# Performance work log

Hardware: AMD Instinct MI355X
Metric: run time of the kernel (lower is better)

The kernel has to match this reference:

```python
import jax, jax.numpy as jnp
import numpy as np

CUTOFF = 0.05

def _freq_filter(x_chw, filter_type):
    # x_chw: [C,H,W] = batch element 0, detached in the original (stop_gradient)
    x = jax.lax.stop_gradient(x_chw)
    C, H, W = x.shape
    a = jnp.abs(x)
    mn = a.min(axis=(1, 2), keepdims=True)
    ptp = a.max(axis=(1, 2), keepdims=True) - mn
    # np.uint8(255*(a-mn)/ptp): values in [0,255], cast truncates -> floor
    q = jnp.floor(255.0 * (a - mn) / ptp)
    f = jnp.fft.fftshift(jnp.fft.fft2(q), axes=(-2, -1))
    crow, ccol = H // 2, W // 2
    dr, dc = int(CUTOFF * crow), int(CUTOFF * ccol)
    m = jnp.zeros((H, W), dtype=q.dtype)
    m = m.at[crow - dr:crow + dr, ccol - dc:ccol + dc].set(1.0)
    if filter_type == 'low_pass':
        m = 1.0 - m  # note: original 'low_pass' actually removes low freqs
    out = jnp.abs(jnp.fft.ifft2(jnp.fft.ifftshift(f * m, axes=(-2, -1))))
    return out.astype(x_chw.dtype)  # [C,H,W]

def _conv1x1(x, w, b):
    # x: [B,C,H,W], w: [O,C], b: [O]
    return jnp.einsum('oc,bchw->bohw', w, x) + b[None, :, None, None]

def setup_inputs() -> dict:
    key = jax.random.key(0)
    ks = jax.random.split(key, 7)
    B, C, H, W = 1, 256, 96, 96
    fuse = jax.random.normal(ks[0], (B, C, H, W), dtype=jnp.float32)
    s = 1.0 / np.sqrt(C)
    Wq = jax.random.normal(ks[1], (C, C), dtype=jnp.float32) * s
    bq = jax.random.normal(ks[2], (C,), dtype=jnp.float32) * 0.01
    Wk = jax.random.normal(ks[3], (C, C), dtype=jnp.float32) * s
    bk = jax.random.normal(ks[4], (C,), dtype=jnp.float32) * 0.01
    Wv = jax.random.normal(ks[5], (C, C), dtype=jnp.float32) * s
    bv = jax.random.normal(ks[6], (C,), dtype=jnp.float32) * 0.01
    return {"fuse": fuse, "Wq": Wq, "bq": bq, "Wk": Wk, "bk": bk, "Wv": Wv, "bv": bv}

def reference(fuse, Wq, bq, Wk, bk, Wv, bv):
    B, C, H, W = fuse.shape
    scale = 1.0 / (C ** 0.5)
    # frequency-filtered maps (computed from batch 0, broadcast to all batches)
    FQ = jnp.broadcast_to(_freq_filter(fuse[0], 'high_pass'), fuse.shape)
    FK = jnp.broadcast_to(_freq_filter(fuse[0], 'low_pass'), fuse.shape)
    fuse_Query = _conv1x1(FQ, Wq, bq).reshape(B, C, H * W)     # [B,C,HW]
    fuse_Q_mask = fuse_Query.reshape(B * H, C * W)             # [B*H, C*W]
    fuse_Query_t = jnp.transpose(fuse_Query, (0, 2, 1))        # [B,HW,C]
    fuse_Key = _conv1x1(FK, Wk, bk).reshape(B, C, H * W)       # [B,C,HW]
    Fuse_Q_mask = jnp.max(fuse_Q_mask, axis=0, keepdims=True)  # [1, C*W]
    mask_KQ = jnp.einsum('bnc,bcm->bnm', fuse_Query_t, fuse_Key) * scale  # [B,HW,HW]
    mask_KQ = jax.nn.softmax(mask_KQ, axis=0)  # softmax over batch dim (as in original)
    mask_KQ = jnp.max(mask_KQ, axis=1)                         # [B,HW]
    mask_KQ = mask_KQ.reshape(-1, W)                           # [B*H, W]
    mask_KQ = jnp.max(mask_KQ, axis=-1, keepdims=True)         # [B*H, 1]
    mask = (mask_KQ @ Fuse_Q_mask).reshape(B, C, H, W)
    fuse_Value = _conv1x1(fuse, Wv, bv)
    return fuse_Value + fuse_Value * mask
```

## Files before the change

### kernel.cpp

```cpp
#include <hip/hip_runtime.h>
#include <math.h>

#define CCH 256
#define HW  9216
#define CW  24576
#define TWO_PI 6.28318530717958647692f

typedef __attribute__((ext_vector_type(8))) short short8;
typedef __attribute__((ext_vector_type(4))) float f32x4;

__device__ inline unsigned short f2bf(float f) {
    unsigned u = __float_as_uint(f);
    unsigned r = (u + 0x7FFFu + ((u >> 16) & 1u)) >> 16;
    return (unsigned short)r;
}

__global__ __launch_bounds__(768) void k_pre(const float* __restrict__ x,
                                             const float* __restrict__ Wq,
                                             const float* __restrict__ Wv,
                                             short8* __restrict__ Wqt,
                                             short8* __restrict__ Wvt,
                                             unsigned* __restrict__ FQm,
                                             float* __restrict__ Fg) {
    __shared__ float qa[HW];
    __shared__ float cs[96][2];
    __shared__ float Gp[8][96][5];
    __shared__ float Gs[96][6];
    __shared__ float red[24];
    __shared__ float s_mn, s_ptp;
    int bid = blockIdx.x, t = threadIdx.x;

    if (bid >= 256) {
        int widx = bid - 256;
        if (t < 256) {
            const float* src = (widx >= 32) ? Wv : Wq;
            short8* dst = (widx >= 32) ? Wvt : Wqt;
            int cidx = (widx & 31) * 256 + t;
            int ot = cidx >> 11, kc = (cidx >> 6) & 31, m = cidx & 63;
            const float* s = src + (ot * 64 + m) * 256 + kc * 8;
            short8 v;
            #pragma unroll
            for (int e = 0; e < 8; ++e) v[e] = (short)f2bf(s[e]);
            dst[cidx] = v;
        }
        return;
    }

    int c = bid;
    if (t < 96) FQm[c * 96 + t] = 0u;
    const float* xp = x + c * HW;
    if (t < 96) { float a = TWO_PI * (float)t / 96.0f; cs[t][0] = cosf(a); cs[t][1] = sinf(a); }
    float lo = 1e30f, hi = 0.f;
    #pragma unroll
    for (int i = 0; i < 12; ++i) {
        float a = fabsf(xp[t + i * 768]);
        qa[t + i * 768] = a;
        lo = fminf(lo, a);
        hi = fmaxf(hi, a);
    }
    #pragma unroll
    for (int d = 32; d; d >>= 1) {
        lo = fminf(lo, __shfl_xor(lo, d, 64));
        hi = fmaxf(hi, __shfl_xor(hi, d, 64));
    }
    if ((t & 63) == 0) { red[t >> 6] = lo; red[12 + (t >> 6)] = hi; }
    __syncthreads();
    if (t == 0) {
        lo = red[0]; hi = red[12];
        #pragma unroll
        for (int i = 1; i < 12; ++i) { lo = fminf(lo, red[i]); hi = fmaxf(hi, red[12 + i]); }
        s_mn = lo; s_ptp = hi - lo;
    }
    __syncthreads();
    float mn = s_mn, ptp = s_ptp;

    {
        int xx = t % 96, h = t / 96;
        float g0r = 0, g0i = 0, g1r = 0, g1i = 0, g2 = 0;
        for (int y = h * 12; y < h * 12 + 12; ++y) {
            float q = floorf(255.0f * (qa[y * 96 + xx] - mn) / ptp);
            float c1 = cs[y][0], s1 = cs[y][1];
            float c2 = c1 * c1 - s1 * s1, s2 = 2.0f * c1 * s1;
            g0r += q * c2; g0i += q * s2;
            g1r += q * c1; g1i += q * s1;
            g2  += q;
        }
        Gp[h][xx][0] = g0r; Gp[h][xx][1] = g0i;
        Gp[h][xx][2] = g1r; Gp[h][xx][3] = g1i;
        Gp[h][xx][4] = g2;
    }
    __syncthreads();
    if (t < 96) {
        #pragma unroll
        for (int j = 0; j < 5; ++j) {
            float s = 0.f;
            #pragma unroll
            for (int h = 0; h < 8; ++h) s += Gp[h][t][j];
            Gs[t][j] = s;
        }
        Gs[t][5] = 0.f;
    }
    __syncthreads();
    if (t < 64) {
        int coef = t >> 2, qq = t & 3;
        int ky = coef >> 2, kx = coef & 3;
        float fr = 0, fi = 0;
        for (int xx = qq * 24; xx < qq * 24 + 24; ++xx) {
            float c1 = cs[xx][0], s1 = cs[xx][1];
            float er, ei;
            if (kx == 0)      { er = c1 * c1 - s1 * s1; ei = 2.0f * c1 * s1; }
            else if (kx == 1) { er = c1; ei = s1; }
            else if (kx == 2) { er = 1.f; ei = 0.f; }
            else              { er = c1; ei = -s1; }
            float gr, gi;
            if (ky == 0)      { gr = Gs[xx][0]; gi = Gs[xx][1]; }
            else if (ky == 1) { gr = Gs[xx][2]; gi = Gs[xx][3]; }
            else if (ky == 2) { gr = Gs[xx][4]; gi = 0.f; }
            else              { gr = Gs[xx][2]; gi = -Gs[xx][3]; }
            fr += gr * er - gi * ei;
            fi += gr * ei + gi * er;
        }
        fr += __shfl_xor(fr, 1, 64); fr += __shfl_xor(fr, 2, 64);
        fi += __shfl_xor(fi, 1, 64); fi += __shfl_xor(fi, 2, 64);
        if (qq == 0) {
            Fg[c * 32 + 2 * coef]     = fr;
            Fg[c * 32 + 2 * coef + 1] = fi;
        }
    }
}

__global__ __launch_bounds__(256) void k_gemm1(const short8* __restrict__ Wt,
                                               const float* __restrict__ Fg,
                                               const float* __restrict__ bias,
                                               unsigned* __restrict__ FQm) {
    __shared__ short8 As[2048];
    __shared__ short8 Bs[2048];
    __shared__ float Rs[2048][2];
    int tid = threadIdx.x;
    int pt_ = blockIdx.x, ot = blockIdx.y;
    const short8* wsrc = Wt + ot * 2048;
    #pragma unroll
    for (int i = 0; i < 8; ++i) As[i * 256 + tid] = wsrc[i * 256 + tid];

    int p0 = pt_ * 64;
    int y0 = p0 / 96;
    {
        int yi = (tid >> 2) & 1, kx = tid & 3, cb = tid >> 3;
        float ay = TWO_PI * (float)(y0 + yi) / 96.0f;
        float cyv = cosf(ay), syv = sinf(ay);
        float cy2 = cyv * cyv - syv * syv, sy2 = 2.f * cyv * syv;
        float Ur[4] = { cy2, cyv, 1.f, cyv };
        float Ui[4] = { -sy2, -syv, 0.f, syv };
        #pragma unroll
        for (int i = 0; i < 8; ++i) {
            int cc = cb + i * 32;
            float rr = 0.f, ri = 0.f;
            #pragma unroll
            for (int ky = 0; ky < 4; ++ky) {
                float fr = Fg[cc * 32 + 2 * (ky * 4 + kx)];
                float fi = Fg[cc * 32 + 2 * (ky * 4 + kx) + 1];
                rr += fr * Ur[ky] - fi * Ui[ky];
                ri += fr * Ui[ky] + fi * Ur[ky];
            }
            Rs[cc * 8 + yi * 4 + kx][0] = rr;
            Rs[cc * 8 + yi * 4 + kx][1] = ri;
        }
    }
    __syncthreads();
    const float inv = 1.0f / 9216.0f;
    #pragma unroll
    for (int i = 0; i < 8; ++i) {
        int si = i * 256 + tid;
        int kcg = si >> 6, n = si & 63;
        int p = p0 + n;
        int y = p / 96, xx = p - y * 96;
        int yi = y - y0;
        float axv = TWO_PI * (float)xx / 96.0f;
        float cxv = cosf(axv), sxv = sinf(axv);
        float cx2 = cxv * cxv - sxv * sxv, sx2 = 2.f * cxv * sxv;
        float Tr[4] = { cx2, cxv, 1.f, cxv };
        float Ti[4] = { -sx2, -sxv, 0.f, sxv };
        short8 vv;
        #pragma unroll
        for (int e = 0; e < 8; ++e) {
            int rb = (kcg * 8 + e) * 8 + yi * 4;
            float ar = 0.f, ai = 0.f;
            #pragma unroll
            for (int kx = 0; kx < 4; ++kx) {
                float rr = Rs[rb + kx][0], ri = Rs[rb + kx][1];
                ar += rr * Tr[kx] - ri * Ti[kx];
                ai += rr * Ti[kx] + ri * Tr[kx];
            }
            vv[e] = (short)f2bf(sqrtf(ar * ar + ai * ai) * inv);
        }
        Bs[si] = vv;
    }
    __syncthreads();

    int l = tid & 63, w = tid >> 6;
    int wr = w >> 1, wc = w & 1;
    int l15 = l & 15, quad = l >> 4;
    f32x4 acc[2][2] = {};
    int abase = wr * 32 + l15;
    int bbase = wc * 32 + l15;
    #pragma unroll
    for (int s = 0; s < 8; ++s) {
        int kc = s * 4 + quad;
        short8 a0 = As[kc * 64 + abase];
        short8 a1 = As[kc * 64 + abase + 16];
        short8 b0 = Bs[kc * 64 + bbase];
        short8 b1 = Bs[kc * 64 + bbase + 16];
        acc[0][0] = __builtin_amdgcn_mfma_f32_16x16x32_bf16(a0, b0, acc[0][0], 0, 0, 0);
        acc[0][1] = __builtin_amdgcn_mfma_f32_16x16x32_bf16(a0, b1, acc[0][1], 0, 0, 0);
        acc[1][0] = __builtin_amdgcn_mfma_f32_16x16x32_bf16(a1, b0, acc[1][0], 0, 0, 0);
        acc[1][1] = __builtin_amdgcn_mfma_f32_16x16x32_bf16(a1, b1, acc[1][1], 0, 0, 0);
    }
    #pragma unroll
    for (int ni = 0; ni < 2; ++ni) {
        #pragma unroll
        for (int r = 0; r < 4; ++r) {
            int o_lo = ot * 64 + wr * 32 + quad * 4 + r;
            float v = fmaxf(acc[0][ni][r] + bias[o_lo], acc[1][ni][r] + bias[o_lo + 16]);
            v = fmaxf(v, __shfl_xor(v, 32, 64));
            if (quad < 2) {
                int p = pt_ * 64 + wc * 32 + ni * 16 + l15;
                int k = ((quad * 4 + r) & 7) * HW + p;
                if (k >= CW) k -= CW;
                if (k >= CW) k -= CW;
                unsigned u = __float_as_uint(v);
                unsigned key = (u & 0x80000000u) ? ~u : (u | 0x80000000u);
                atomicMax(&FQm[k], key);
            }
        }
    }
}

__global__ __launch_bounds__(256) void k_gemm2(const short8* __restrict__ Wt,
                                               const float* __restrict__ x,
                                               const float* __restrict__ bias,
                                               const unsigned* __restrict__ FQm,
                                               float* __restrict__ out) {
    __shared__ short8 As[2048];
    __shared__ short8 Bs[2048];
    int tid = threadIdx.x;
    int pt_ = blockIdx.x, ot = blockIdx.y;
    const short8* wsrc = Wt + ot * 2048;
    #pragma unroll
    for (int i = 0; i < 8; ++i) As[i * 256 + tid] = wsrc[i * 256 + tid];

    int p0 = pt_ * 64;
    #pragma unroll
    for (int i = 0; i < 8; ++i) {
        int si = i * 256 + tid;
        int KC = si >> 6, n = si & 63;
        const float* xb = x + (size_t)(KC * 8) * HW + p0 + n;
        short8 v;
        #pragma unroll
        for (int e = 0; e < 8; ++e) v[e] = (short)f2bf(xb[(size_t)e * HW]);
        Bs[si] = v;
    }
    __syncthreads();

    int l = tid & 63, w = tid >> 6;
    int wr = w >> 1, wc = w & 1;
    int l15 = l & 15, quad = l >> 4;
    f32x4 acc[2][2] = {};
    int abase = wr * 32 + l15;
    int bbase = wc * 32 + l15;
    #pragma unroll
    for (int s = 0; s < 8; ++s) {
        int kc = s * 4 + quad;
        short8 a0 = As[kc * 64 + abase];
        short8 a1 = As[kc * 64 + abase + 16];
        short8 b0 = Bs[kc * 64 + bbase];
        short8 b1 = Bs[kc * 64 + bbase + 16];
        acc[0][0] = __builtin_amdgcn_mfma_f32_16x16x32_bf16(a0, b0, acc[0][0], 0, 0, 0);
        acc[0][1] = __builtin_amdgcn_mfma_f32_16x16x32_bf16(a0, b1, acc[0][1], 0, 0, 0);
        acc[1][0] = __builtin_amdgcn_mfma_f32_16x16x32_bf16(a1, b0, acc[1][0], 0, 0, 0);
        acc[1][1] = __builtin_amdgcn_mfma_f32_16x16x32_bf16(a1, b1, acc[1][1], 0, 0, 0);
    }
    #pragma unroll
    for (int mi = 0; mi < 2; ++mi) {
        #pragma unroll
        for (int ni = 0; ni < 2; ++ni) {
            #pragma unroll
            for (int r = 0; r < 4; ++r) {
                int o = ot * 64 + wr * 32 + mi * 16 + quad * 4 + r;
                int p = pt_ * 64 + wc * 32 + ni * 16 + l15;
                int k = ((quad * 4 + r) & 7) * HW + p;
                if (k >= CW) k -= CW;
                if (k >= CW) k -= CW;
                unsigned key = FQm[k];
                unsigned ub = (key & 0x80000000u) ? (key ^ 0x80000000u) : ~key;
                float m = __uint_as_float(ub);
                float v = acc[mi][ni][r] + bias[o];
                out[(size_t)o * HW + p] = v * (1.0f + m);
            }
        }
    }
}

extern "C" void kernel_launch(void* const* d_in, const int* in_sizes, int n_in,
                              void* d_out, int out_size, void* d_ws, size_t ws_size,
                              hipStream_t stream) {
    const float* fuse = (const float*)d_in[0];
    const float* Wq   = (const float*)d_in[1];
    const float* bq   = (const float*)d_in[2];
    const float* Wv   = (const float*)d_in[5];
    const float* bv   = (const float*)d_in[6];
    float* out = (float*)d_out;

    char* ws = (char*)d_ws;
    unsigned* FQm = (unsigned*)(ws);
    float*    Fg  = (float*)(ws + 98304);
    short8*   Wqt = (short8*)(ws + 131072);
    short8*   Wvt = (short8*)(ws + 262144);

    k_pre<<<320, 768, 0, stream>>>(fuse, Wq, Wv, Wqt, Wvt, FQm, Fg);
    k_gemm1<<<dim3(144, 4), 256, 0, stream>>>(Wqt, Fg, bq, FQm);
    k_gemm2<<<dim3(144, 4), 256, 0, stream>>>(Wvt, fuse, bv, FQm, out);
}
```

Baseline: 115.6 us.

## Merge Q and V GEMMs into one launch and apply mask in separate pass

Fuses the Q-projection GEMM (with FFT reconstruction and atomic max) and the V-projection GEMM into a single 1152-block launch, so both run concurrently instead of V waiting for Q. Because V blocks can no longer read the finished mask, they write the unmasked value to the output, and a new elementwise kernel then reads the output back, applies the mask and writes it again. The aim is better GPU fill and one fewer serialized GEMM dependency. The cost is an extra read and write pass over the roughly 9 MB output, plus one more kernel launch.

```diff
diff --git a/kernel.cpp b/kernel.cpp
--- a/kernel.cpp
+++ b/kernel.cpp
@@ -129,71 +129,90 @@
     }
 }
 
-__global__ __launch_bounds__(256) void k_gemm1(const short8* __restrict__ Wt,
-                                               const float* __restrict__ Fg,
-                                               const float* __restrict__ bias,
-                                               unsigned* __restrict__ FQm) {
+__global__ __launch_bounds__(256) void k_gemmQV(const short8* __restrict__ Wqt,
+                                                const short8* __restrict__ Wvt,
+                                                const float* __restrict__ Fg,
+                                                const float* __restrict__ bq,
+                                                const float* __restrict__ bv,
+                                                const float* __restrict__ x,
+                                                unsigned* __restrict__ FQm,
+                                                float* __restrict__ out) {
     __shared__ short8 As[2048];
     __shared__ short8 Bs[2048];
     __shared__ float Rs[2048][2];
     int tid = threadIdx.x;
-    int pt_ = blockIdx.x, ot = blockIdx.y;
-    const short8* wsrc = Wt + ot * 2048;
+    int pt_ = blockIdx.x;
+    bool isQ = blockIdx.y < 4;
+    int ot = isQ ? blockIdx.y : blockIdx.y - 4;
+    const short8* wsrc = (isQ ? Wqt : Wvt) + ot * 2048;
     #pragma unroll
     for (int i = 0; i < 8; ++i) As[i * 256 + tid] = wsrc[i * 256 + tid];
 
     int p0 = pt_ * 64;
-    int y0 = p0 / 96;
-    {
-        int yi = (tid >> 2) & 1, kx = tid & 3, cb = tid >> 3;
-        float ay = TWO_PI * (float)(y0 + yi) / 96.0f;
-        float cyv = cosf(ay), syv = sinf(ay);
-        float cy2 = cyv * cyv - syv * syv, sy2 = 2.f * cyv * syv;
-        float Ur[4] = { cy2, cyv, 1.f, cyv };
-        float Ui[4] = { -sy2, -syv, 0.f, syv };
+    if (isQ) {
+        int y0 = p0 / 96;
+        {
+            int yi = (tid >> 2) & 1, kx = tid & 3, cb = tid >> 3;
+            float ay = TWO_PI * (float)(y0 + yi) / 96.0f;
+            float cyv = cosf(ay), syv = sinf(ay);
+            float cy2 = cyv * cyv - syv * syv, sy2 = 2.f * cyv * syv;
+            float Ur[4] = { cy2, cyv, 1.f, cyv };
+            float Ui[4] = { -sy2, -syv, 0.f, syv };
+            #pragma unroll
+            for (int i = 0; i < 8; ++i) {
+                int cc = cb + i * 32;
+                float rr = 0.f, ri = 0.f;
+                #pragma unroll
+                for (int ky = 0; ky < 4; ++ky) {
+                    float fr = Fg[cc * 32 + 2 * (ky * 4 + kx)];
+                    float fi = Fg[cc * 32 + 2 * (ky * 4 + kx) + 1];
+                    rr += fr * Ur[ky] - fi * Ui[ky];
+                    ri += fr * Ui[ky] + fi * Ur[ky];
+                }
+                Rs[cc * 8 + yi * 4 + kx][0] = rr;
+                Rs[cc * 8 + yi * 4 + kx][1] = ri;
+            }
+        }
+        __syncthreads();
+        const float inv = 1.0f / 9216.0f;
         #pragma unroll
         for (int i = 0; i < 8; ++i) {
-            int cc = cb + i * 32;
-            float rr = 0.f, ri = 0.f;
-            #pragma unroll
-            for (int ky = 0; ky < 4; ++ky) {
-                float fr = Fg[cc * 32 + 2 * (ky * 4 + kx)];
-                float fi = Fg[cc * 32 + 2 * (ky * 4 + kx) + 1];
-                rr += fr * Ur[ky] - fi * Ui[ky];
-                ri += fr * Ui[ky] + fi * Ur[ky];
+            int si = i * 256 + tid;
+            int kcg = si >> 6, n = si & 63;
+            int p = p0 + n;
+            int y = p / 96, xx = p - y * 96;
+            int yi = y - y0;
+            float axv = TWO_PI * (float)xx / 96.0f;
+            float cxv = cosf(axv), sxv = sinf(axv);
+            float cx2 = cxv * cxv - sxv * sxv, sx2 = 2.f * cxv * sxv;
+            float Tr[4] = { cx2, cxv, 1.f, cxv };
+            float Ti[4] = { -sx2, -sxv, 0.f, sxv };
+            short8 vv;
+            #pragma unroll
+            for (int e = 0; e < 8; ++e) {
+                int rb = (kcg * 8 + e) * 8 + yi * 4;
+                float ar = 0.f, ai = 0.f;
+                #pragma unroll
+                for (int kx = 0; kx < 4; ++kx) {
+                    float rr = Rs[rb + kx][0], ri = Rs[rb + kx][1];
+                    ar += rr * Tr[kx] - ri * Ti[kx];
+                    ai += rr * Ti[kx] + ri * Tr[kx];
+                }
+                vv[e] = (short)f2bf(sqrtf(ar * ar + ai * ai) * inv);
             }
-            Rs[cc * 8 + yi * 4 + kx][0] = rr;
-            Rs[cc * 8 + yi * 4 + kx][1] = ri;
-        }
-    }
-    __syncthreads();
-    const float inv = 1.0f / 9216.0f;
-    #pragma unroll
-    for (int i = 0; i < 8; ++i) {
-        int si = i * 256 + tid;
-        int kcg = si >> 6, n = si & 63;
-        int p = p0 + n;
-        int y = p / 96, xx = p - y * 96;
-        int yi = y - y0;
-        float axv = TWO_PI * (float)xx / 96.0f;
-        float cxv = cosf(axv), sxv = sinf(axv);
-        float cx2 = cxv * cxv - sxv * sxv, sx2 = 2.f * cxv * sxv;
-        float Tr[4] = { cx2, cxv, 1.f, cxv };
-        float Ti[4] = { -sx2, -sxv, 0.f, sxv };
-        short8 vv;
-        #pragma unroll
-        for (int e = 0; e < 8; ++e) {
-            int rb = (kcg * 8 + e) * 8 + yi * 4;
-            float ar = 0.f, ai = 0.f;
-            #pragma unroll
-            for (int kx = 0; kx < 4; ++kx) {
-                float rr = Rs[rb + kx][0], ri = Rs[rb + kx][1];
-                ar += rr * Tr[kx] - ri * Ti[kx];
-                ai += rr * Ti[kx] + ri * Tr[kx];
-            }
-            vv[e] = (short)f2bf(sqrtf(ar * ar + ai * ai) * inv);
-        }
-        Bs[si] = vv;
+            Bs[si] = vv;
+        }
+    } else {
+        #pragma unroll
+        for (int i = 0; i < 8; ++i) {
+            int si = i * 256 + tid;
+            int KC = si >> 6, n = si & 63;
+            const float* xb = x + (size_t)(KC * 8) * HW + p0 + n;
+            short8 v;
+            #pragma unroll
+            for (int e = 0; e < 8; ++e) v[e] = (short)f2bf(xb[(size_t)e * HW]);
+            Bs[si] = v;
+        }
     }
     __syncthreads();
 
@@ -215,89 +234,64 @@
         acc[1][0] = __builtin_amdgcn_mfma_f32_16x16x32_bf16(a1, b0, acc[1][0], 0, 0, 0);
         acc[1][1] = __builtin_amdgcn_mfma_f32_16x16x32_bf16(a1, b1, acc[1][1], 0, 0, 0);
     }
-    #pragma unroll
-    for (int ni = 0; ni < 2; ++ni) {
-        #pragma unroll
-        for (int r = 0; r < 4; ++r) {
-            int o_lo = ot * 64 + wr * 32 + quad * 4 + r;
-            float v = fmaxf(acc[0][ni][r] + bias[o_lo], acc[1][ni][r] + bias[o_lo + 16]);
-            v = fmaxf(v, __shfl_xor(v, 32, 64));
-            if (quad < 2) {
-                int p = pt_ * 64 + wc * 32 + ni * 16 + l15;
-                int k = ((quad * 4 + r) & 7) * HW + p;
-                if (k >= CW) k -= CW;
-                if (k >= CW) k -= CW;
-                unsigned u = __float_as_uint(v);
-                unsigned key = (u & 0x80000000u) ? ~u : (u | 0x80000000u);
-                atomicMax(&FQm[k], key);
+
+    if (isQ) {
+        #pragma unroll
+        for (int ni = 0; ni < 2; ++ni) {
+            #pragma unroll
+            for (int r = 0; r < 4; ++r) {
+                int o_lo = ot * 64 + wr * 32 + quad * 4 + r;
+                float v = fmaxf(acc[0][ni][r] + bq[o_lo], acc[1][ni][r] + bq[o_lo + 16]);
+                v = fmaxf(v, __shfl_xor(v, 32, 64));
+                if (quad < 2) {
+                    int p = pt_ * 64 + wc * 32 + ni * 16 + l15;
+                    int k = ((quad * 4 + r) & 7) * HW + p;
+                    if (k >= CW) k -= CW;
+                    if (k >= CW) k -= CW;
+                    unsigned u = __float_as_uint(v);
+                    unsigned key = (u & 0x80000000u) ? ~u : (u | 0x80000000u);
+                    atomicMax(&FQm[k], key);
+                }
             }
         }
-    }
-}
-
-__global__ __launch_bounds__(256) void k_gemm2(const short8* __restrict__ Wt,
-                                               const float* __restrict__ x,
-                                               const float* __restrict__ bias,
-                                               const unsigned* __restrict__ FQm,
-                                               float* __restrict__ out) {
-    __shared__ short8 As[2048];
-    __shared__ short8 Bs[2048];
-    int tid = threadIdx.x;
-    int pt_ = blockIdx.x, ot = blockIdx.y;
-    const short8* wsrc = Wt + ot * 2048;
-    #pragma unroll
-    for (int i = 0; i < 8; ++i) As[i * 256 + tid] = wsrc[i * 256 + tid];
-
-    int p0 = pt_ * 64;
-    #pragma unroll
-    for (int i = 0; i < 8; ++i) {
-        int si = i * 256 + tid;
-        int KC = si >> 6, n = si & 63;
-        const float* xb = x + (size_t)(KC * 8) * HW + p0 + n;
-        short8 v;
-        #pragma unroll
-        for (int e = 0; e < 8; ++e) v[e] = (short)f2bf(xb[(size_t)e * HW]);
-        Bs[si] = v;
-    }
-    __syncthreads();
-
-    int l = tid & 63, w = tid >> 6;
-    int wr = w >> 1, wc = w & 1;
-    int l15 = l & 15, quad = l >> 4;
-    f32x4 acc[2][2] = {};
-    int abase = wr * 32 + l15;
-    int bbase = wc * 32 + l15;
-    #pragma unroll
-    for (int s = 0; s < 8; ++s) {
-        int kc = s * 4 + quad;
-        short8 a0 = As[kc * 64 + abase];
-        short8 a1 = As[kc * 64 + abase + 16];
-        short8 b0 = Bs[kc * 64 + bbase];
-        short8 b1 = Bs[kc * 64 + bbase + 16];
-        acc[0][0] = __builtin_amdgcn_mfma_f32_16x16x32_bf16(a0, b0, acc[0][0], 0, 0, 0);
-        acc[0][1] = __builtin_amdgcn_mfma_f32_16x16x32_bf16(a0, b1, acc[0][1], 0, 0, 0);
-        acc[1][0] = __builtin_amdgcn_mfma_f32_16x16x32_bf16(a1, b0, acc[1][0], 0, 0, 0);
-        acc[1][1] = __builtin_amdgcn_mfma_f32_16x16x32_bf16(a1, b1, acc[1][1], 0, 0, 0);
-    }
-    #pragma unroll
-    for (int mi = 0; mi < 2; ++mi) {
-        #pragma unroll
-        for (int ni = 0; ni < 2; ++ni) {
-            #pragma unroll
-            for (int r = 0; r < 4; ++r) {
-                int o = ot * 64 + wr * 32 + mi * 16 + quad * 4 + r;
-                int p = pt_ * 64 + wc * 32 + ni * 16 + l15;
-                int k = ((quad * 4 + r) & 7) * HW + p;
-                if (k >= CW) k -= CW;
-                if (k >= CW) k -= CW;
-                unsigned key = FQm[k];
-                unsigned ub = (key & 0x80000000u) ? (key ^ 0x80000000u) : ~key;
-                float m = __uint_as_float(ub);
-                float v = acc[mi][ni][r] + bias[o];
-                out[(size_t)o * HW + p] = v * (1.0f + m);
+    } else {
+        #pragma unroll
+        for (int mi = 0; mi < 2; ++mi) {
+            #pragma unroll
+            for (int ni = 0; ni < 2; ++ni) {
+                #pragma unroll
+                for (int r = 0; r < 4; ++r) {
+                    int o = ot * 64 + wr * 32 + mi * 16 + quad * 4 + r;
+                    int p = pt_ * 64 + wc * 32 + ni * 16 + l15;
+                    out[(size_t)o * HW + p] = acc[mi][ni][r] + bv[o];
+                }
             }
         }
     }
+}
+
+__device__ inline float mdecode(unsigned key) {
+    unsigned ub = (key & 0x80000000u) ? (key ^ 0x80000000u) : ~key;
+    return __uint_as_float(ub);
+}
+__global__ __launch_bounds__(256) void k_mask(float* __restrict__ out,
+                                              const unsigned* __restrict__ FQm) {
+    int i = (blockIdx.x * 256 + threadIdx.x) * 8;
+    int o = i / HW;
+    int p = i - o * HW;
+    int k = (o & 7) * HW + p;
+    if (k >= CW) k -= CW;
+    if (k >= CW) k -= CW;
+    float4 v0 = *(const float4*)(out + i);
+    float4 v1 = *(const float4*)(out + i + 4);
+    uint4 k0 = *(const uint4*)(FQm + k);
+    uint4 k1 = *(const uint4*)(FQm + k + 4);
+    v0.x *= 1.0f + mdecode(k0.x); v0.y *= 1.0f + mdecode(k0.y);
+    v0.z *= 1.0f + mdecode(k0.z); v0.w *= 1.0f + mdecode(k0.w);
+    v1.x *= 1.0f + mdecode(k1.x); v1.y *= 1.0f + mdecode(k1.y);
+    v1.z *= 1.0f + mdecode(k1.z); v1.w *= 1.0f + mdecode(k1.w);
+    *(float4*)(out + i)     = v0;
+    *(float4*)(out + i + 4) = v1;
 }
 
 extern "C" void kernel_launch(void* const* d_in, const int* in_sizes, int n_in,
@@ -317,6 +311,6 @@
     short8*   Wvt = (short8*)(ws + 262144);
 
     k_pre<<<320, 768, 0, stream>>>(fuse, Wq, Wv, Wqt, Wvt, FQm, Fg);
-    k_gemm1<<<dim3(144, 4), 256, 0, stream>>>(Wqt, Fg, bq, FQm);
-    k_gemm2<<<dim3(144, 4), 256, 0, stream>>>(Wvt, fuse, bv, FQm, out);
-}
+    k_gemmQV<<<dim3(144, 8), 256, 0, stream>>>(Wqt, Wvt, Fg, bq, bv, fuse, FQm, out);
+    k_mask<<<1152, 256, 0, stream>>>(out, FQm);
+}
```

After: 114.1 us, median of 3. About the same (-1.2%).

## Fuse three kernels into one cooperative persistent kernel with grid syncs

Applied to the files above, without the earlier changes.

Merges the preprocessing, Q-conv mask GEMM and V-conv output GEMM into a single cooperative kernel. Grid-wide syncs separate the phases, and blocks loop over tasks and tiles. The goal is to remove two kernel launch gaps. The preprocessing block shrinks from 768 to 256 threads, so each channel's spectral reduction runs with fewer threads per block. In exchange it adds grid.sync overhead, a fixed grid size, and a per-call occupancy query on the host.

```diff
diff --git a/kernel.cpp b/kernel.cpp
--- a/kernel.cpp
+++ b/kernel.cpp
@@ -1,300 +1,284 @@
 #include <hip/hip_runtime.h>
+#include <hip/hip_cooperative_groups.h>
 #include <math.h>
 
-#define CCH 256
 #define HW  9216
 #define CW  24576
 #define TWO_PI 6.28318530717958647692f
 
+namespace cg = cooperative_groups;
+
 typedef __attribute__((ext_vector_type(8))) short short8;
 typedef __attribute__((ext_vector_type(4))) float f32x4;
 
 __device__ inline unsigned short f2bf(float f) {
     unsigned u = __float_as_uint(f);
-    unsigned r = (u + 0x7FFFu + ((u >> 16) & 1u)) >> 16;
-    return (unsigned short)r;
+    return (unsigned short)((u + 0x7FFFu + ((u >> 16) & 1u)) >> 16);
 }
 
-__global__ __launch_bounds__(768) void k_pre(const float* __restrict__ x,
-                                             const float* __restrict__ Wq,
-                                             const float* __restrict__ Wv,
-                                             short8* __restrict__ Wqt,
-                                             short8* __restrict__ Wvt,
-                                             unsigned* __restrict__ FQm,
-                                             float* __restrict__ Fg) {
-    __shared__ float qa[HW];
-    __shared__ float cs[96][2];
-    __shared__ float Gp[8][96][5];
-    __shared__ float Gs[96][6];
-    __shared__ float red[24];
-    __shared__ float s_mn, s_ptp;
-    int bid = blockIdx.x, t = threadIdx.x;
-
-    if (bid >= 256) {
-        int widx = bid - 256;
-        if (t < 256) {
-            const float* src = (widx >= 32) ? Wv : Wq;
-            short8* dst = (widx >= 32) ? Wvt : Wqt;
-            int cidx = (widx & 31) * 256 + t;
-            int ot = cidx >> 11, kc = (cidx >> 6) & 31, m = cidx & 63;
-            const float* s = src + (ot * 64 + m) * 256 + kc * 8;
+__global__ __launch_bounds__(256, 2) void k_all(const float* __restrict__ x,
+                                                const float* __restrict__ Wq,
+                                                const float* __restrict__ Wv,
+                                                const float* __restrict__ bq,
+                                                const float* __restrict__ bv,
+                                                unsigned* __restrict__ FQm,
+                                                float* __restrict__ Fg,
+                                                short8* __restrict__ Wqt,
+                                                short8* __restrict__ Wvt,
+                                                float* __restrict__ out) {
+    __shared__ __align__(16) char smem[81920];
+    cg::grid_group grid = cg::this_grid();
+    const int bid = blockIdx.x, t = threadIdx.x;
+    const int G = gridDim.x;
+
+    for (int task = bid; task < 368; task += G) {
+        if (task < 256) {
+            float* qa        = (float*)smem;
+            float (*cs)[2]   = (float(*)[2])(smem + 36864);
+            float (*Gp)[96][5] = (float(*)[96][5])(smem + 37632);
+            float (*Gs)[6]   = (float(*)[6])(smem + 41472);
+            float* red       = (float*)(smem + 43776);
+            const float* xp = x + task * HW;
+            if (t < 96) { float a = TWO_PI * (float)t / 96.0f; cs[t][0] = cosf(a); cs[t][1] = sinf(a); }
+            float lo = 1e30f, hi = 0.f;
+            #pragma unroll
+            for (int i = 0; i < 36; ++i) {
+                float a = fabsf(xp[t + i * 256]);
+                qa[t + i * 256] = a;
+                lo = fminf(lo, a); hi = fmaxf(hi, a);
+            }
+            #pragma unroll
+            for (int d = 32; d; d >>= 1) {
+                lo = fminf(lo, __shfl_xor(lo, d, 64));
+                hi = fmaxf(hi, __shfl_xor(hi, d, 64));
+            }
+            if ((t & 63) == 0) { red[t >> 6] = lo; red[4 + (t >> 6)] = hi; }
+            __syncthreads();
+            if (t == 0) {
+                lo = fminf(fminf(red[0], red[1]), fminf(red[2], red[3]));
+                hi = fmaxf(fmaxf(red[4], red[5]), fmaxf(red[6], red[7]));
+                red[8] = lo; red[9] = hi - lo;
+            }
+            __syncthreads();
+            float mn = red[8], ptp = red[9];
+            if (t < 192) {
+                int xx = t % 96, h = t / 96;
+                float g0r = 0, g0i = 0, g1r = 0, g1i = 0, g2 = 0;
+                for (int y = h * 48; y < h * 48 + 48; ++y) {
+                    float q = floorf(255.0f * (qa[y * 96 + xx] - mn) / ptp);
+                    float c1 = cs[y][0], s1 = cs[y][1];
+                    float c2 = c1 * c1 - s1 * s1, s2 = 2.0f * c1 * s1;
+                    g0r += q * c2; g0i += q * s2;
+                    g1r += q * c1; g1i += q * s1;
+                    g2  += q;
+                }
+                Gp[h][xx][0] = g0r; Gp[h][xx][1] = g0i;
+                Gp[h][xx][2] = g1r; Gp[h][xx][3] = g1i;
+                Gp[h][xx][4] = g2;
+            }
+            __syncthreads();
+            if (t < 96) {
+                #pragma unroll
+                for (int j = 0; j < 5; ++j) Gs[t][j] = Gp[0][t][j] + Gp[1][t][j];
+                Gs[t][5] = 0.f;
+            }
+            __syncthreads();
+            if (t < 64) {
+                int coef = t >> 2, qq = t & 3;
+                int ky = coef >> 2, kx = coef & 3;
+                float fr = 0, fi = 0;
+                for (int xx = qq * 24; xx < qq * 24 + 24; ++xx) {
+                    float c1 = cs[xx][0], s1 = cs[xx][1];
+                    float er, ei;
+                    if (kx == 0)      { er = c1 * c1 - s1 * s1; ei = 2.0f * c1 * s1; }
+                    else if (kx == 1) { er = c1; ei = s1; }
+                    else if (kx == 2) { er = 1.f; ei = 0.f; }
+                    else              { er = c1; ei = -s1; }
+                    float gr, gi;
+                    if (ky == 0)      { gr = Gs[xx][0]; gi = Gs[xx][1]; }
+                    else if (ky == 1) { gr = Gs[xx][2]; gi = Gs[xx][3]; }
+                    else if (ky == 2) { gr = Gs[xx][4]; gi = 0.f; }
+                    else              { gr = Gs[xx][2]; gi = -Gs[xx][3]; }
+                    fr += gr * er - gi * ei;
+                    fi += gr * ei + gi * er;
+                }
+                fr += __shfl_xor(fr, 1, 64); fr += __shfl_xor(fr, 2, 64);
+                fi += __shfl_xor(fi, 1, 64); fi += __shfl_xor(fi, 2, 64);
+                if (qq == 0) {
+                    Fg[task * 32 + 2 * coef]     = fr;
+                    Fg[task * 32 + 2 * coef + 1] = fi;
+                }
+            }
+            __syncthreads();
+        } else if (task < 272) {
+            int gi = (task - 256) * 256 + t;
+            #pragma unroll
+            for (int r = 0; r < 4; ++r) {
+                int chunk = gi + r * 4096;
+                const float* src = (chunk < 8192) ? Wq : Wv;
+                short8* dst = (chunk < 8192) ? Wqt : Wvt;
+                int cidx = chunk & 8191;
+                int ot = cidx >> 11, kc = (cidx >> 6) & 31, m = cidx & 63;
+                const float* s = src + (ot * 64 + m) * 256 + kc * 8;
+                short8 v;
+                #pragma unroll
+                for (int e = 0; e < 8; ++e) v[e] = (short)f2bf(s[e]);
+                dst[cidx] = v;
+            }
+        } else {
+            FQm[(task - 272) * 256 + t] = 0u;
+        }
+    }
+    grid.sync();
+
+    short8* As = (short8*)smem;
+    short8* Bs = (short8*)(smem + 32768);
+    float (*Rs)[2] = (float(*)[2])(smem + 65536);
+    const int l = t & 63, w = t >> 6;
+    const int wr = w >> 1, wc = w & 1;
+    const int l15 = l & 15, quad = l >> 4;
+    const int abase = wr * 32 + l15, bbase = wc * 32 + l15;
+
+    for (int tile = bid; tile < 576; tile += G) {
+        __syncthreads();
+        int ot = tile / 144, pt_ = tile % 144;
+        const short8* wsrc = Wqt + ot * 2048;
+        #pragma unroll
+        for (int i = 0; i < 8; ++i) As[i * 256 + t] = wsrc[i * 256 + t];
+        int p0 = pt_ * 64, y0 = p0 / 96;
+        {
+            int yi = (t >> 2) & 1, kx = t & 3, cb = t >> 3;
+            float ay = TWO_PI * (float)(y0 + yi) / 96.0f;
+            float cyv = cosf(ay), syv = sinf(ay);
+            float cy2 = cyv * cyv - syv * syv, sy2 = 2.f * cyv * syv;
+            float Ur[4] = { cy2, cyv, 1.f, cyv };
+            float Ui[4] = { -sy2, -syv, 0.f, syv };
+            #pragma unroll
+            for (int i = 0; i < 8; ++i) {
+                int cc = cb + i * 32;
+                float rr = 0.f, ri = 0.f;
+                #pragma unroll
+                for (int ky = 0; ky < 4; ++ky) {
+                    float fr = Fg[cc * 32 + 2 * (ky * 4 + kx)];
+                    float fi = Fg[cc * 32 + 2 * (ky * 4 + kx) + 1];
+                    rr += fr * Ur[ky] - fi * Ui[ky];
+                    ri += fr * Ui[ky] + fi * Ur[ky];
+                }
+                Rs[cc * 8 + yi * 4 + kx][0] = rr;
+                Rs[cc * 8 + yi * 4 + kx][1] = ri;
+            }
+        }
+        __syncthreads();
+        const float inv = 1.0f / 9216.0f;
+        #pragma unroll
+        for (int i = 0; i < 8; ++i) {
+            int si = i * 256 + t;
+            int kcg = si >> 6, n = si & 63;
+            int p = p0 + n;
+            int y = p / 96, xx = p - y * 96;
+            int yi = y - y0;
+            float axv = TWO_PI * (float)xx / 96.0f;
+            float cxv = cosf(axv), sxv = sinf(axv);
+            float cx2 = cxv * cxv - sxv * sxv, sx2 = 2.f * cxv * sxv;
+            float Tr[4] = { cx2, cxv, 1.f, cxv };
+            float Ti[4] = { -sx2, -sxv, 0.f, sxv };
+            short8 vv;
+            #pragma unroll
+            for (int e = 0; e < 8; ++e) {
+                int rb = (kcg * 8 + e) * 8 + yi * 4;
+                float ar = 0.f, ai = 0.f;
+                #pragma unroll
+                for (int kx2 = 0; kx2 < 4; ++kx2) {
+                    float rr = Rs[rb + kx2][0], ri = Rs[rb + kx2][1];
+                    ar += rr * Tr[kx2] - ri * Ti[kx2];
+                    ai += rr * Ti[kx2] + ri * Tr[kx2];
+                }
+                vv[e] = (short)f2bf(sqrtf(ar * ar + ai * ai) * inv);
+            }
+            Bs[si] = vv;
+        }
+        __syncthreads();
+        f32x4 acc[2][2] = {};
+        #pragma unroll
+        for (int s = 0; s < 8; ++s) {
+            int kc = s * 4 + quad;
+            short8 a0 = As[kc * 64 + abase];
+            short8 a1 = As[kc * 64 + abase + 16];
+            short8 b0 = Bs[kc * 64 + bbase];
+            short8 b1 = Bs[kc * 64 + bbase + 16];
+            acc[0][0] = __builtin_amdgcn_mfma_f32_16x16x32_bf16(a0, b0, acc[0][0], 0, 0, 0);
+            acc[0][1] = __builtin_amdgcn_mfma_f32_16x16x32_bf16(a0, b1, acc[0][1], 0, 0, 0);
+            acc[1][0] = __builtin_amdgcn_mfma_f32_16x16x32_bf16(a1, b0, acc[1][0], 0, 0, 0);
+            acc[1][1] = __builtin_amdgcn_mfma_f32_16x16x32_bf16(a1, b1, acc[1][1], 0, 0, 0);
+        }
+        #pragma unroll
+        for (int ni = 0; ni < 2; ++ni) {
+            #pragma unroll
+            for (int r = 0; r < 4; ++r) {
+                int o_lo = ot * 64 + wr * 32 + quad * 4 + r;
+                float v = fmaxf(acc[0][ni][r] + bq[o_lo], acc[1][ni][r] + bq[o_lo + 16]);
+                v = fmaxf(v, __shfl_xor(v, 32, 64));
+                if (quad < 2) {
+                    int p = pt_ * 64 + wc * 32 + ni * 16 + l15;
+                    int k = ((quad * 4 + r) & 7) * HW + p;
+                    if (k >= CW) k -= CW;
+                    if (k >= CW) k -= CW;
+                    unsigned u = __float_as_uint(v);
+                    unsigned key = (u & 0x80000000u) ? ~u : (u | 0x80000000u);
+                    atomicMax(&FQm[k], key);
+                }
+            }
+        }
+    }
+    grid.sync();
+
+    for (int tile = bid; tile < 576; tile += G) {
+        __syncthreads();
+        int ot = tile / 144, pt_ = tile % 144;
+        const short8* wsrc = Wvt + ot * 2048;
+        #pragma unroll
+        for (int i = 0; i < 8; ++i) As[i * 256 + t] = wsrc[i * 256 + t];
+        int p0 = pt_ * 64;
+        #pragma unroll
+        for (int i = 0; i < 8; ++i) {
+            int si = i * 256 + t;
+            int KC = si >> 6, n = si & 63;
+            const float* xb = x + (size_t)(KC * 8) * HW + p0 + n;
             short8 v;
             #pragma unroll
-            for (int e = 0; e < 8; ++e) v[e] = (short)f2bf(s[e]);
-            dst[cidx] = v;
-        }
-        return;
-    }
-
-    int c = bid;
-    if (t < 96) FQm[c * 96 + t] = 0u;
-    const float* xp = x + c * HW;
-    if (t < 96) { float a = TWO_PI * (float)t / 96.0f; cs[t][0] = cosf(a); cs[t][1] = sinf(a); }
-    float lo = 1e30f, hi = 0.f;
-    #pragma unroll
-    for (int i = 0; i < 12; ++i) {
-        float a = fabsf(xp[t + i * 768]);
-        qa[t + i * 768] = a;
-        lo = fminf(lo, a);
-        hi = fmaxf(hi, a);
-    }
-    #pragma unroll
-    for (int d = 32; d; d >>= 1) {
-        lo = fminf(lo, __shfl_xor(lo, d, 64));
-        hi = fmaxf(hi, __shfl_xor(hi, d, 64));
-    }
-    if ((t & 63) == 0) { red[t >> 6] = lo; red[12 + (t >> 6)] = hi; }
-    __syncthreads();
-    if (t == 0) {
-        lo = red[0]; hi = red[12];
-        #pragma unroll
-        for (int i = 1; i < 12; ++i) { lo = fminf(lo, red[i]); hi = fmaxf(hi, red[12 + i]); }
-        s_mn = lo; s_ptp = hi - lo;
-    }
-    __syncthreads();
-    float mn = s_mn, ptp = s_ptp;
-
-    {
-        int xx = t % 96, h = t / 96;
-        float g0r = 0, g0i = 0, g1r = 0, g1i = 0, g2 = 0;
-        for (int y = h * 12; y < h * 12 + 12; ++y) {
-            float q = floorf(255.0f * (qa[y * 96 + xx] - mn) / ptp);
-            float c1 = cs[y][0], s1 = cs[y][1];
-            float c2 = c1 * c1 - s1 * s1, s2 = 2.0f * c1 * s1;
-            g0r += q * c2; g0i += q * s2;
-            g1r += q * c1; g1i += q * s1;
-            g2  += q;
-        }
-        Gp[h][xx][0] = g0r; Gp[h][xx][1] = g0i;
-        Gp[h][xx][2] = g1r; Gp[h][xx][3] = g1i;
-        Gp[h][xx][4] = g2;
-    }
-    __syncthreads();
-    if (t < 96) {
-        #pragma unroll
-        for (int j = 0; j < 5; ++j) {
-            float s = 0.f;
-            #pragma unroll
-            for (int h = 0; h < 8; ++h) s += Gp[h][t][j];
-            Gs[t][j] = s;
-        }
-        Gs[t][5] = 0.f;
-    }
-    __syncthreads();
-    if (t < 64) {
-        int coef = t >> 2, qq = t & 3;
-        int ky = coef >> 2, kx = coef & 3;
-        float fr = 0, fi = 0;
-        for (int xx = qq * 24; xx < qq * 24 + 24; ++xx) {
-            float c1 = cs[xx][0], s1 = cs[xx][1];
-            float er, ei;
-            if (kx == 0)      { er = c1 * c1 - s1 * s1; ei = 2.0f * c1 * s1; }
-            else if (kx == 1) { er = c1; ei = s1; }
-            else if (kx == 2) { er = 1.f; ei = 0.f; }
-            else              { er = c1; ei = -s1; }
-            float gr, gi;
-            if (ky == 0)      { gr = Gs[xx][0]; gi = Gs[xx][1]; }
-            else if (ky == 1) { gr = Gs[xx][2]; gi = Gs[xx][3]; }
-            else if (ky == 2) { gr = Gs[xx][4]; gi = 0.f; }
-            else              { gr = Gs[xx][2]; gi = -Gs[xx][3]; }
-            fr += gr * er - gi * ei;
-            fi += gr * ei + gi * er;
-        }
-        fr += __shfl_xor(fr, 1, 64); fr += __shfl_xor(fr, 2, 64);
-        fi += __shfl_xor(fi, 1, 64); fi += __shfl_xor(fi, 2, 64);
-        if (qq == 0) {
-            Fg[c * 32 + 2 * coef]     = fr;
-            Fg[c * 32 + 2 * coef + 1] = fi;
-        }
-    }
-}
-
-__global__ __launch_bounds__(256) void k_gemm1(const short8* __restrict__ Wt,
-                                               const float* __restrict__ Fg,
-                                               const float* __restrict__ bias,
-                                               unsigned* __restrict__ FQm) {
-    __shared__ short8 As[2048];
-    __shared__ short8 Bs[2048];
-    __shared__ float Rs[2048][2];
-    int tid = threadIdx.x;
-    int pt_ = blockIdx.x, ot = blockIdx.y;
-    const short8* wsrc = Wt + ot * 2048;
-    #pragma unroll
-    for (int i = 0; i < 8; ++i) As[i * 256 + tid] = wsrc[i * 256 + tid];
-
-    int p0 = pt_ * 64;
-    int y0 = p0 / 96;
-    {
-        int yi = (tid >> 2) & 1, kx = tid & 3, cb = tid >> 3;
-        float ay = TWO_PI * (float)(y0 + yi) / 96.0f;
-        float cyv = cosf(ay), syv = sinf(ay);
-        float cy2 = cyv * cyv - syv * syv, sy2 = 2.f * cyv * syv;
-        float Ur[4] = { cy2, cyv, 1.f, cyv };
-        float Ui[4] = { -sy2, -syv, 0.f, syv };
-        #pragma unroll
-        for (int i = 0; i < 8; ++i) {
-            int cc = cb + i * 32;
-            float rr = 0.f, ri = 0.f;
-            #pragma unroll
-            for (int ky = 0; ky < 4; ++ky) {
-                float fr = Fg[cc * 32 + 2 * (ky * 4 + kx)];
-                float fi = Fg[cc * 32 + 2 * (ky * 4 + kx) + 1];
-                rr += fr * Ur[ky] - fi * Ui[ky];
-                ri += fr * Ui[ky] + fi * Ur[ky];
-            }
-            Rs[cc * 8 + yi * 4 + kx][0] = rr;
-            Rs[cc * 8 + yi * 4 + kx][1] = ri;
-        }
-    }
-    __syncthreads();
-    const float inv = 1.0f / 9216.0f;
-    #pragma unroll
-    for (int i = 0; i < 8; ++i) {
-        int si = i * 256 + tid;
-        int kcg = si >> 6, n = si & 63;
-        int p = p0 + n;
-        int y = p / 96, xx = p - y * 96;
-        int yi = y - y0;
-        float axv = TWO_PI * (float)xx / 96.0f;
-        float cxv = cosf(axv), sxv = sinf(axv);
-        float cx2 = cxv * cxv - sxv * sxv, sx2 = 2.f * cxv * sxv;
-        float Tr[4] = { cx2, cxv, 1.f, cxv };
-        float Ti[4] = { -sx2, -sxv, 0.f, sxv };
-        short8 vv;
-        #pragma unroll
-        for (int e = 0; e < 8; ++e) {
-            int rb = (kcg * 8 + e) * 8 + yi * 4;
-            float ar = 0.f, ai = 0.f;
-            #pragma unroll
-            for (int kx = 0; kx < 4; ++kx) {
-                float rr = Rs[rb + kx][0], ri = Rs[rb + kx][1];
-                ar += rr * Tr[kx] - ri * Ti[kx];
-                ai += rr * Ti[kx] + ri * Tr[kx];
-            }
-            vv[e] = (short)f2bf(sqrtf(ar * ar + ai * ai) * inv);
-        }
-        Bs[si] = vv;
-    }
-    __syncthreads();
-
-    int l = tid & 63, w = tid >> 6;
-    int wr = w >> 1, wc = w & 1;
-    int l15 = l & 15, quad = l >> 4;
-    f32x4 acc[2][2] = {};
-    int abase = wr * 32 + l15;
-    int bbase = wc * 32 + l15;
-    #pragma unroll
-    for (int s = 0; s < 8; ++s) {
-        int kc = s * 4 + quad;
-        short8 a0 = As[kc * 64 + abase];
-        short8 a1 = As[kc * 64 + abase + 16];
-        short8 b0 = Bs[kc * 64 + bbase];
-        short8 b1 = Bs[kc * 64 + bbase + 16];
-        acc[0][0] = __builtin_amdgcn_mfma_f32_16x16x32_bf16(a0, b0, acc[0][0], 0, 0, 0);
-        acc[0][1] = __builtin_amdgcn_mfma_f32_16x16x32_bf16(a0, b1, acc[0][1], 0, 0, 0);
-        acc[1][0] = __builtin_amdgcn_mfma_f32_16x16x32_bf16(a1, b0, acc[1][0], 0, 0, 0);
-        acc[1][1] = __builtin_amdgcn_mfma_f32_16x16x32_bf16(a1, b1, acc[1][1], 0, 0, 0);
-    }
-    #pragma unroll
-    for (int ni = 0; ni < 2; ++ni) {
-        #pragma unroll
-        for (int r = 0; r < 4; ++r) {
-            int o_lo = ot * 64 + wr * 32 + quad * 4 + r;
-            float v = fmaxf(acc[0][ni][r] + bias[o_lo], acc[1][ni][r] + bias[o_lo + 16]);
-            v = fmaxf(v, __shfl_xor(v, 32, 64));
-            if (quad < 2) {
-                int p = pt_ * 64 + wc * 32 + ni * 16 + l15;
-                int k = ((quad * 4 + r) & 7) * HW + p;
-                if (k >= CW) k -= CW;
-                if (k >= CW) k -= CW;
-                unsigned u = __float_as_uint(v);
-                unsigned key = (u & 0x80000000u) ? ~u : (u | 0x80000000u);
-                atomicMax(&FQm[k], key);
-            }
-        }
-    }
-}
-
-__global__ __launch_bounds__(256) void k_gemm2(const short8* __restrict__ Wt,
-                                               const float* __restrict__ x,
-                                               const float* __restrict__ bias,
-                                               const unsigned* __restrict__ FQm,
-                                               float* __restrict__ out) {
-    __shared__ short8 As[2048];
-    __shared__ short8 Bs[2048];
-    int tid = threadIdx.x;
-    int pt_ = blockIdx.x, ot = blockIdx.y;
-    const short8* wsrc = Wt + ot * 2048;
-    #pragma unroll
-    for (int i = 0; i < 8; ++i) As[i * 256 + tid] = wsrc[i * 256 + tid];
-
-    int p0 = pt_ * 64;
-    #pragma unroll
-    for (int i = 0; i < 8; ++i) {
-        int si = i * 256 + tid;
-        int KC = si >> 6, n = si & 63;
-        const float* xb = x + (size_t)(KC * 8) * HW + p0 + n;
-        short8 v;
-        #pragma unroll
-        for (int e = 0; e < 8; ++e) v[e] = (short)f2bf(xb[(size_t)e * HW]);
-        Bs[si] = v;
-    }
-    __syncthreads();
-
-    int l = tid & 63, w = tid >> 6;
-    int wr = w >> 1, wc = w & 1;
-    int l15 = l & 15, quad = l >> 4;
-    f32x4 acc[2][2] = {};
-    int abase = wr * 32 + l15;
-    int bbase = wc * 32 + l15;
-    #pragma unroll
-    for (int s = 0; s < 8; ++s) {
-        int kc = s * 4 + quad;
-        short8 a0 = As[kc * 64 + abase];
-        short8 a1 = As[kc * 64 + abase + 16];
-        short8 b0 = Bs[kc * 64 + bbase];
-        short8 b1 = Bs[kc * 64 + bbase + 16];
-        acc[0][0] = __builtin_amdgcn_mfma_f32_16x16x32_bf16(a0, b0, acc[0][0], 0, 0, 0);
-        acc[0][1] = __builtin_amdgcn_mfma_f32_16x16x32_bf16(a0, b1, acc[0][1], 0, 0, 0);
-        acc[1][0] = __builtin_amdgcn_mfma_f32_16x16x32_bf16(a1, b0, acc[1][0], 0, 0, 0);
-        acc[1][1] = __builtin_amdgcn_mfma_f32_16x16x32_bf16(a1, b1, acc[1][1], 0, 0, 0);
-    }
-    #pragma unroll
-    for (int mi = 0; mi < 2; ++mi) {
-        #pragma unroll
-        for (int ni = 0; ni < 2; ++ni) {
-            #pragma unroll
-            for (int r = 0; r < 4; ++r) {
-                int o = ot * 64 + wr * 32 + mi * 16 + quad * 4 + r;
-                int p = pt_ * 64 + wc * 32 + ni * 16 + l15;
-                int k = ((quad * 4 + r) & 7) * HW + p;
-                if (k >= CW) k -= CW;
-                if (k >= CW) k -= CW;
-                unsigned key = FQm[k];
-                unsigned ub = (key & 0x80000000u) ? (key ^ 0x80000000u) : ~key;
-                float m = __uint_as_float(ub);
-                float v = acc[mi][ni][r] + bias[o];
-                out[(size_t)o * HW + p] = v * (1.0f + m);
+            for (int e = 0; e < 8; ++e) v[e] = (short)f2bf(xb[(size_t)e * HW]);
+            Bs[si] = v;
+        }
+        __syncthreads();
+        f32x4 acc[2][2] = {};
+        #pragma unroll
+        for (int s = 0; s < 8; ++s) {
+            int kc = s * 4 + quad;
+            short8 a0 = As[kc * 64 + abase];
+            short8 a1 = As[kc * 64 + abase + 16];
+            short8 b0 = Bs[kc * 64 + bbase];
+            short8 b1 = Bs[kc * 64 + bbase + 16];
+            acc[0][0] = __builtin_amdgcn_mfma_f32_16x16x32_bf16(a0, b0, acc[0][0], 0, 0, 0);
+            acc[0][1] = __builtin_amdgcn_mfma_f32_16x16x32_bf16(a0, b1, acc[0][1], 0, 0, 0);
+            acc[1][0] = __builtin_amdgcn_mfma_f32_16x16x32_bf16(a1, b0, acc[1][0], 0, 0, 0);
+            acc[1][1] = __builtin_amdgcn_mfma_f32_16x16x32_bf16(a1, b1, acc[1][1], 0, 0, 0);
+        }
+        #pragma unroll
+        for (int mi = 0; mi < 2; ++mi) {
+            #pragma unroll
+            for (int ni = 0; ni < 2; ++ni) {
+                #pragma unroll
+                for (int r = 0; r < 4; ++r) {
+                    int o = ot * 64 + wr * 32 + mi * 16 + quad * 4 + r;
+                    int p = pt_ * 64 + wc * 32 + ni * 16 + l15;
+                    int k = ((quad * 4 + r) & 7) * HW + p;
+                    if (k >= CW) k -= CW;
+                    if (k >= CW) k -= CW;
+                    unsigned key = FQm[k];
+                    unsigned ub = (key & 0x80000000u) ? (key ^ 0x80000000u) : ~key;
+                    float m = __uint_as_float(ub);
+                    out[(size_t)o * HW + p] = (acc[mi][ni][r] + bv[o]) * (1.0f + m);
+                }
             }
         }
     }
@@ -316,7 +300,13 @@
     short8*   Wqt = (short8*)(ws + 131072);
     short8*   Wvt = (short8*)(ws + 262144);
 
-    k_pre<<<320, 768, 0, stream>>>(fuse, Wq, Wv, Wqt, Wvt, FQm, Fg);
-    k_gemm1<<<dim3(144, 4), 256, 0, stream>>>(Wqt, Fg, bq, FQm);
-    k_gemm2<<<dim3(144, 4), 256, 0, stream>>>(Wvt, fuse, bv, FQm, out);
+    int occ = 2;
+    hipOccupancyMaxActiveBlocksPerMultiprocessor(&occ, k_all, 256, 0);
+    int G = occ * 256;
+    if (G > 512) G = 512;
+    if (G < 1)   G = 256;
+
+    void* args[] = { (void*)&fuse, (void*)&Wq, (void*)&Wv, (void*)&bq, (void*)&bv,
+                     (void*)&FQm, (void*)&Fg, (void*)&Wqt, (void*)&Wvt, (void*)&out };
+    hipLaunchCooperativeKernel((void*)k_all, dim3(G), dim3(256), args, 0, stream);
 }
```

Result: slower. 198.1 us (+71.4%).
